# Performance work log

Hardware: AMD Instinct MI355X
Metric: run time of the kernel (lower is better)

## Reference

```python
import jax, jax.numpy as jnp
import numpy as np

B, K, HID, EMB = 16384, 8, 512, 512


def setup_inputs() -> dict:
    key = jax.random.key(0)
    ks = jax.random.split(key, 6)
    scale = 1.0 / np.sqrt(HID)
    return {
        "query": jax.random.normal(ks[0], (B, HID), jnp.float32),
        "topics": jax.random.normal(ks[1], (B, K, EMB), jnp.float32),
        "coverage_vector": jax.random.uniform(ks[2], (B, K), jnp.float32),
        "Ua_w": jax.random.normal(ks[3], (HID, EMB), jnp.float32) * scale,
        "Wa_w": jax.random.normal(ks[4], (HID, HID), jnp.float32) * scale,
        "va_w": jax.random.normal(ks[5], (HID,), jnp.float32) * scale,
        "va_b": jnp.zeros((1,), jnp.float32),
    }


def reference(query, topics, coverage_vector, Ua_w, Wa_w, va_w, va_b):
    # Faithful to the torch loop: query is re-projected by Wa EACH step,
    # so step i uses Wa^(i+1)(query) -- a sequential recurrence over K topics.
    # proj_key for all topics can be batched: [B,K,EMB] @ Ua_w.T -> [B,K,HID]
    proj_key = jnp.einsum('bke,he->bkh', topics, Ua_w)

    def step(q, pk_i):
        # q: [B,HID]; pk_i: [B,HID] (proj_key for topic i)
        q_new = q @ Wa_w.T
        s = jnp.tanh(q_new + pk_i) @ va_w + va_b[0]  # [B]
        return q_new, s

    # scan over the K topic steps (carry = evolving query)
    _, scores = jax.lax.scan(step, query, jnp.moveaxis(proj_key, 1, 0))
    scores = scores.T * coverage_vector  # [B,K]
    alphas = jax.nn.softmax(scores, axis=1)
    mt = jnp.einsum('bk,bke->be', alphas, topics)
    return mt, alphas
```

## Files before the change

kernel.cpp:

```cpp
#include <hip/hip_runtime.h>
#include <hip/hip_bf16.h>

#define HID 512
#define EMB 512
#define KTOP 8
#define BM 64
#define THREADS 1024
#define POWN (512 * 512)

typedef __attribute__((ext_vector_type(8))) short bf16x8;
typedef __attribute__((ext_vector_type(4))) float f32x4;
typedef __attribute__((ext_vector_type(4))) unsigned u32x4;

__device__ __forceinline__ short f2bf(float f) {
    unsigned u = __builtin_bit_cast(unsigned, f);
    u += 0x7fffu + ((u >> 16) & 1u);
    return (short)(u >> 16);
}
__device__ __forceinline__ float bf2f(short s) {
    unsigned u = ((unsigned)(unsigned short)s) << 16;
    return __builtin_bit_cast(float, u);
}
__device__ __forceinline__ unsigned cvtpk2(float x, float y) {
    return ((unsigned)(unsigned short)f2bf(x)) |
           (((unsigned)(unsigned short)f2bf(y)) << 16);
}
__device__ __forceinline__ bf16x8 pack8(f32x4 a, f32x4 b) {
    u32x4 r = {cvtpk2(a[0], a[1]), cvtpk2(a[2], a[3]),
               cvtpk2(b[0], b[1]), cvtpk2(b[2], b[3])};
    return __builtin_bit_cast(bf16x8, r);
}
__device__ __forceinline__ void split_bf(float w, short& hi, short& lo) {
    hi = f2bf(w);
    lo = f2bf(w - bf2f(hi));
}

__global__ void prep_kernel(const float* __restrict__ Wa, const float* __restrict__ Ua,
                            short* __restrict__ hiRM, short* __restrict__ loRM,
                            short* __restrict__ hiT, short* __restrict__ loT,
                            short* __restrict__ ua_b) {
    int i = blockIdx.x * blockDim.x + threadIdx.x;
    if (i >= POWN) return;
    int r = i >> 9, c = i & 511;
    short hi, lo;
    split_bf(Wa[i], hi, lo);
    hiRM[i] = hi; loRM[i] = lo;
    hiT[c * 512 + r] = hi;
    loT[c * 512 + r] = lo;
    ua_b[i] = f2bf(Ua[i]);
}

__device__ __forceinline__ int sel4(int4 v, int i) {
    int r = v.x;
    if (i == 1) r = v.y;
    if (i == 2) r = v.z;
    if (i == 3) r = v.w;
    return r;
}

__global__ __launch_bounds__(256)
void powmul_kernel(short* __restrict__ hiRM, short* __restrict__ loRM,
                   short* __restrict__ hiT, short* __restrict__ loT,
                   int4 aS, int4 bS, int4 dS) {
    const int p = blockIdx.z;
    const int as = sel4(aS, p), bs = sel4(bS, p), ds = sel4(dS, p);
    const short* Ah = hiRM + (size_t)as * POWN;
    const short* Al = loRM + (size_t)as * POWN;
    const short* Bh = hiT + (size_t)bs * POWN;
    const short* Bl = loT + (size_t)bs * POWN;

    const int tid = threadIdx.x, lane = tid & 63, w = tid >> 6;
    const int l15 = lane & 15, lg = lane >> 4;
    const int row = blockIdx.x * 64 + w * 16 + l15;
    const int colb = blockIdx.y * 64;

    f32x4 acc[4];
#pragma unroll
    for (int nf = 0; nf < 4; ++nf) acc[nf] = (f32x4){0.f, 0.f, 0.f, 0.f};

    for (int ch = 0; ch < 16; ++ch) {
        const int e0 = ch * 32 + lg * 8;
        bf16x8 ah = *(const bf16x8*)(Ah + row * 512 + e0);
        bf16x8 al = *(const bf16x8*)(Al + row * 512 + e0);
#pragma unroll
        for (int nf = 0; nf < 4; ++nf) {
            const int col = colb + nf * 16 + l15;
            bf16x8 bh = *(const bf16x8*)(Bh + col * 512 + e0);
            bf16x8 bl = *(const bf16x8*)(Bl + col * 512 + e0);
            acc[nf] = __builtin_amdgcn_mfma_f32_16x16x32_bf16(ah, bh, acc[nf], 0, 0, 0);
            acc[nf] = __builtin_amdgcn_mfma_f32_16x16x32_bf16(ah, bl, acc[nf], 0, 0, 0);
            acc[nf] = __builtin_amdgcn_mfma_f32_16x16x32_bf16(al, bh, acc[nf], 0, 0, 0);
        }
    }

    short* Dh = hiRM + (size_t)ds * POWN;
    short* Dl = loRM + (size_t)ds * POWN;
#pragma unroll
    for (int nf = 0; nf < 4; ++nf)
#pragma unroll
        for (int j = 0; j < 4; ++j) {
            int rg = blockIdx.x * 64 + w * 16 + lg * 4 + j;
            int cg = colb + nf * 16 + l15;
            short hi, lo;
            split_bf(acc[nf][j], hi, lo);
            Dh[rg * 512 + cg] = hi;
            Dl[rg * 512 + cg] = lo;
            if (ds < 4) {
                hiT[(size_t)ds * POWN + cg * 512 + rg] = hi;
                loT[(size_t)ds * POWN + cg * 512 + rg] = lo;
            }
        }
}

__global__ __launch_bounds__(256)
void swz_pow_kernel(const short* __restrict__ pow_hi, const short* __restrict__ pow_lo,
                    const short* __restrict__ ua_b,
                    short* __restrict__ swz_hi, short* __restrict__ swz_lo,
                    short* __restrict__ swz_ua) {
    const int m = blockIdx.y;
    const short* src;
    short* dst;
    if (m < 8)       { src = pow_hi + (size_t)m * POWN;       dst = swz_hi + (size_t)m * POWN; }
    else if (m < 16) { src = pow_lo + (size_t)(m - 8) * POWN; dst = swz_lo + (size_t)(m - 8) * POWN; }
    else             { src = ua_b;                             dst = swz_ua; }

#pragma unroll
    for (int i = 0; i < 8; ++i) {
        int c = blockIdx.x * 2048 + i * 256 + threadIdx.x;
        bf16x8 v = *(const bf16x8*)(src + c * 8);
        int ch = (c >> 2) & 15;
        int lg = c & 3;
        int cb = c >> 10;
        int l15 = (c >> 6) & 15;
        int lane = lg * 16 + l15;
        *(bf16x8*)(dst + ((size_t)(ch * 32 + cb) * 64 + lane) * 8) = v;
    }
}

__global__ __launch_bounds__(THREADS)
void q_prep_kernel(const float* __restrict__ query, short* __restrict__ q_sw) {
    __shared__ short q_s[BM * 512];
    const int tid = threadIdx.x;
    const long rbase = (long)blockIdx.x * BM;

#pragma unroll
    for (int i = 0; i < 4; ++i) {
        int idx = tid + i * THREADS;
        int r = idx >> 6, s = idx & 63;
        const float* qp = query + (rbase + r) * HID + s * 8;
        f32x4 a = *(const f32x4*)qp;
        f32x4 b = *(const f32x4*)(qp + 4);
        *(bf16x8*)&q_s[(r * 64 + (s ^ (r & 7))) * 8] = pack8(a, b);
    }
    __syncthreads();
    short* dst = q_sw + (size_t)blockIdx.x * (BM * 512);
#pragma unroll
    for (int i = 0; i < 4; ++i) {
        int d = tid + i * THREADS;
        int l15 = d & 15, lg = (d >> 4) & 3;
        int ch = (d >> 6) & 15, mf = (d >> 10) & 3;
        int r = mf * 16 + l15;
        int s = ch * 4 + lg;
        bf16x8 v = *(const bf16x8*)&q_s[(r * 64 + (s ^ (r & 7))) * 8];
        *(bf16x8*)(dst + (size_t)d * 8) = v;
    }
}

__global__ __launch_bounds__(THREADS, 4)
void attn_main_kernel(const float* __restrict__ topics,
                      const float* __restrict__ cov,
                      const short* __restrict__ q_sw,
                      const short* __restrict__ swz_hi,
                      const short* __restrict__ swz_lo,
                      const short* __restrict__ swz_ua,
                      const float* __restrict__ va_w,
                      const float* __restrict__ va_b,
                      float* __restrict__ out_mt,
                      float* __restrict__ out_alpha) {
    __shared__ short t_lds[BM * 512];
    __shared__ float scores_s[BM][KTOP];
    __shared__ float alpha_s[BM][KTOP];

    const int tid  = threadIdx.x;
    const int lane = tid & 63;
    const int wn   = tid >> 6;
    const int l15  = lane & 15;
    const int lg   = lane >> 4;
    const long rbase = (long)blockIdx.x * BM;

    if (tid < BM * KTOP) ((float*)scores_s)[tid] = 0.f;

    float va_reg[2];
#pragma unroll
    for (int nf = 0; nf < 2; ++nf) va_reg[nf] = va_w[wn * 32 + nf * 16 + l15];
    const float vab = va_b[0];

    const short* qbase = q_sw + (size_t)blockIdx.x * (BM * 512) + lane * 8;
    const int lane8 = lane * 8;

#pragma unroll 1
    for (int step = 0; step < KTOP; ++step) {
        __syncthreads();
#pragma unroll
        for (int i = 0; i < 4; ++i) {
            int idx = tid + i * THREADS;
            int r = idx >> 6, s = idx & 63;
            const float* tp = topics + ((rbase + r) * KTOP + step) * EMB + s * 8;
            f32x4 a = *(const f32x4*)tp;
            f32x4 b = *(const f32x4*)(tp + 4);
            *(bf16x8*)&t_lds[(r * 64 + (s ^ (r & 7))) * 8] = pack8(a, b);
        }
        __syncthreads();

        const short* wh = swz_hi + (size_t)step * POWN;
        const short* wl = swz_lo + (size_t)step * POWN;

        f32x4 acc[4][2];
#pragma unroll
        for (int mf = 0; mf < 4; ++mf)
#pragma unroll
            for (int nf = 0; nf < 2; ++nf) acc[mf][nf] = (f32x4){0.f, 0.f, 0.f, 0.f};

        for (int ch = 0; ch < 16; ++ch) {
            bf16x8 qf[4], tf[4];
#pragma unroll
            for (int mf = 0; mf < 4; ++mf) {
                qf[mf] = *(const bf16x8*)(qbase + (size_t)(mf * 16 + ch) * 512);
                int r = mf * 16 + l15;
                int s = ch * 4 + lg;
                tf[mf] = *(const bf16x8*)&t_lds[(r * 64 + (s ^ (r & 7))) * 8];
            }
#pragma unroll
            for (int nf = 0; nf < 2; ++nf) {
                const size_t off = (size_t)((ch * 32 + wn * 2 + nf) * 512 + lane8);
                bf16x8 bh = *(const bf16x8*)(wh + off);
                bf16x8 bl = *(const bf16x8*)(wl + off);
                bf16x8 bu = *(const bf16x8*)(swz_ua + off);
#pragma unroll
                for (int mf = 0; mf < 4; ++mf) {
                    acc[mf][nf] = __builtin_amdgcn_mfma_f32_16x16x32_bf16(qf[mf], bh, acc[mf][nf], 0, 0, 0);
                    acc[mf][nf] = __builtin_amdgcn_mfma_f32_16x16x32_bf16(qf[mf], bl, acc[mf][nf], 0, 0, 0);
                    acc[mf][nf] = __builtin_amdgcn_mfma_f32_16x16x32_bf16(tf[mf], bu, acc[mf][nf], 0, 0, 0);
                }
            }
        }

        float part[4][4];
#pragma unroll
        for (int mf = 0; mf < 4; ++mf)
#pragma unroll
            for (int j = 0; j < 4; ++j) part[mf][j] = 0.f;
#pragma unroll
        for (int mf = 0; mf < 4; ++mf)
#pragma unroll
            for (int nf = 0; nf < 2; ++nf)
#pragma unroll
                for (int j = 0; j < 4; ++j) {
                    float x = acc[mf][nf][j];
                    float e = __expf(2.f * x);
                    float th = 1.f - 2.f / (e + 1.f);
                    part[mf][j] += th * va_reg[nf];
                }
#pragma unroll
        for (int m = 8; m >= 1; m >>= 1)
#pragma unroll
            for (int mf = 0; mf < 4; ++mf)
#pragma unroll
                for (int j = 0; j < 4; ++j)
                    part[mf][j] += __shfl_xor(part[mf][j], m, 64);
        if (l15 == 0) {
#pragma unroll
            for (int mf = 0; mf < 4; ++mf)
#pragma unroll
                for (int j = 0; j < 4; ++j)
                    atomicAdd(&scores_s[mf * 16 + lg * 4 + j][step], part[mf][j]);
        }
    }

    __syncthreads();
    if (tid < BM * KTOP) {
        int r = tid >> 3, k = tid & 7;
        scores_s[r][k] = (scores_s[r][k] + vab) * cov[(rbase + r) * KTOP + k];
    }
    __syncthreads();
    if (tid < BM) {
        float mx = scores_s[tid][0];
#pragma unroll
        for (int k = 1; k < KTOP; ++k) mx = fmaxf(mx, scores_s[tid][k]);
        float e[KTOP], sum = 0.f;
#pragma unroll
        for (int k = 0; k < KTOP; ++k) { e[k] = __expf(scores_s[tid][k] - mx); sum += e[k]; }
#pragma unroll
        for (int k = 0; k < KTOP; ++k) {
            float a = e[k] / sum;
            alpha_s[tid][k] = a;
            out_alpha[(rbase + tid) * KTOP + k] = a;
        }
    }
    __syncthreads();

#pragma unroll 1
    for (int i = tid; i < BM * (EMB / 4); i += THREADS) {
        int r = i >> 7;
        int c4 = i & 127;
        const float* tb = topics + (rbase + r) * KTOP * EMB + c4 * 4;
        f32x4 acc = {0.f, 0.f, 0.f, 0.f};
#pragma unroll
        for (int k = 0; k < KTOP; ++k) {
            f32x4 t = *(const f32x4*)(tb + k * EMB);
            float a = alpha_s[r][k];
            acc[0] += t[0] * a;
            acc[1] += t[1] * a;
            acc[2] += t[2] * a;
            acc[3] += t[3] * a;
        }
        *(f32x4*)(out_mt + (rbase + r) * EMB + c4 * 4) = acc;
    }
}

extern "C" void kernel_launch(void* const* d_in, const int* in_sizes, int n_in,
                              void* d_out, int out_size, void* d_ws, size_t ws_size,
                              hipStream_t stream) {
    const float* query  = (const float*)d_in[0];
    const float* topics = (const float*)d_in[1];
    const float* cov    = (const float*)d_in[2];
    const float* Ua     = (const float*)d_in[3];
    const float* Wa     = (const float*)d_in[4];
    const float* va     = (const float*)d_in[5];
    const float* vab    = (const float*)d_in[6];

    const int Brows = in_sizes[0] / HID;
    const int nblk  = Brows / BM;

    short* pow_hi = (short*)d_ws;
    short* pow_lo = pow_hi + (size_t)8 * POWN;
    short* hiT    = pow_lo + (size_t)8 * POWN;
    short* loT    = hiT + (size_t)4 * POWN;
    short* ua_b   = loT + (size_t)4 * POWN;
    short* swz_hi = ua_b + POWN;
    short* swz_lo = swz_hi + (size_t)8 * POWN;
    short* swz_ua = swz_lo + (size_t)8 * POWN;
    short* q_sw   = swz_ua + POWN;

    float* out_mt    = (float*)d_out;
    float* out_alpha = out_mt + (size_t)Brows * EMB;

    prep_kernel<<<(POWN + 255) / 256, 256, 0, stream>>>(Wa, Ua, pow_hi, pow_lo,
                                                        hiT, loT, ua_b);
    powmul_kernel<<<dim3(8, 8, 1), 256, 0, stream>>>(pow_hi, pow_lo, hiT, loT,
        make_int4(0, 0, 0, 0), make_int4(0, 0, 0, 0), make_int4(1, 0, 0, 0));
    powmul_kernel<<<dim3(8, 8, 2), 256, 0, stream>>>(pow_hi, pow_lo, hiT, loT,
        make_int4(1, 1, 0, 0), make_int4(0, 1, 0, 0), make_int4(2, 3, 0, 0));
    powmul_kernel<<<dim3(8, 8, 4), 256, 0, stream>>>(pow_hi, pow_lo, hiT, loT,
        make_int4(3, 3, 2, 3), make_int4(0, 1, 3, 3), make_int4(4, 5, 6, 7));

    swz_pow_kernel<<<dim3(16, 17), 256, 0, stream>>>(pow_hi, pow_lo, ua_b,
                                                     swz_hi, swz_lo, swz_ua);
    q_prep_kernel<<<nblk, THREADS, 0, stream>>>(query, q_sw);

    attn_main_kernel<<<nblk, THREADS, 0, stream>>>(topics, cov, q_sw,
                                                   swz_hi, swz_lo, swz_ua,
                                                   va, vab, out_mt, out_alpha);
}
```

Before: 401.3 us.

## Double-buffer topic tiles and fuse online-softmax weighted sum into step loop

Topic tiles for the next step are prefetched into registers while the current step's MFMA work runs, then written to a second LDS buffer. The final mt computation no longer re-reads all topics from global memory. Instead, an online-softmax running sum over the bf16 topic tile already in LDS is kept in 32 registers per thread. This saves a full second pass over the topics tensor, but mt is now built from bf16-rounded topics, which costs accuracy. It also doubles LDS use and adds registers, which may hurt occupancy.

```diff
diff --git a/kernel.cpp b/kernel.cpp
--- a/kernel.cpp
+++ b/kernel.cpp
@@ -177,9 +177,8 @@
                       const float* __restrict__ va_b,
                       float* __restrict__ out_mt,
                       float* __restrict__ out_alpha) {
-    __shared__ short t_lds[BM * 512];
+    __shared__ short t_lds[2][BM * 512];
     __shared__ float scores_s[BM][KTOP];
-    __shared__ float alpha_s[BM][KTOP];
 
     const int tid  = threadIdx.x;
     const int lane = tid & 63;
@@ -195,22 +194,44 @@
     for (int nf = 0; nf < 2; ++nf) va_reg[nf] = va_w[wn * 32 + nf * 16 + l15];
     const float vab = va_b[0];
 
+    const int orow = tid >> 4;
+    const int oc0  = (tid & 15) * 32;
+    float o_acc[32];
+#pragma unroll
+    for (int j = 0; j < 32; ++j) o_acc[j] = 0.f;
+    float l_run = 0.f, m_run = -1e30f;
+
     const short* qbase = q_sw + (size_t)blockIdx.x * (BM * 512) + lane * 8;
     const int lane8 = lane * 8;
 
-#pragma unroll 1
-    for (int step = 0; step < KTOP; ++step) {
-        __syncthreads();
+    f32x4 sa[4], sb[4];
+    auto issue_stage = [&](int stp) {
 #pragma unroll
         for (int i = 0; i < 4; ++i) {
             int idx = tid + i * THREADS;
             int r = idx >> 6, s = idx & 63;
-            const float* tp = topics + ((rbase + r) * KTOP + step) * EMB + s * 8;
-            f32x4 a = *(const f32x4*)tp;
-            f32x4 b = *(const f32x4*)(tp + 4);
-            *(bf16x8*)&t_lds[(r * 64 + (s ^ (r & 7))) * 8] = pack8(a, b);
-        }
-        __syncthreads();
+            const float* tp = topics + ((rbase + r) * KTOP + stp) * EMB + s * 8;
+            sa[i] = *(const f32x4*)tp;
+            sb[i] = *(const f32x4*)(tp + 4);
+        }
+    };
+    auto write_stage = [&](int buf) {
+#pragma unroll
+        for (int i = 0; i < 4; ++i) {
+            int idx = tid + i * THREADS;
+            int r = idx >> 6, s = idx & 63;
+            *(bf16x8*)&t_lds[buf][(r * 64 + (s ^ (r & 7))) * 8] = pack8(sa[i], sb[i]);
+        }
+    };
+
+    issue_stage(0);
+    write_stage(0);
+    __syncthreads();
+
+#pragma unroll 1
+    for (int step = 0; step < KTOP; ++step) {
+        const int cur = step & 1;
+        if (step < KTOP - 1) issue_stage(step + 1);
 
         const short* wh = swz_hi + (size_t)step * POWN;
         const short* wl = swz_lo + (size_t)step * POWN;
@@ -228,7 +249,7 @@
                 qf[mf] = *(const bf16x8*)(qbase + (size_t)(mf * 16 + ch) * 512);
                 int r = mf * 16 + l15;
                 int s = ch * 4 + lg;
-                tf[mf] = *(const bf16x8*)&t_lds[(r * 64 + (s ^ (r & 7))) * 8];
+                tf[mf] = *(const bf16x8*)&t_lds[cur][(r * 64 + (s ^ (r & 7))) * 8];
             }
 #pragma unroll
             for (int nf = 0; nf < 2; ++nf) {
@@ -275,9 +296,32 @@
                 for (int j = 0; j < 4; ++j)
                     atomicAdd(&scores_s[mf * 16 + lg * 4 + j][step], part[mf][j]);
         }
-    }
-
-    __syncthreads();
+
+        __syncthreads();
+
+        {
+            float cv  = cov[(rbase + orow) * KTOP + step];
+            float s_k = (scores_s[orow][step] + vab) * cv;
+            float m_new = fmaxf(m_run, s_k);
+            float corr = __expf(m_run - m_new);
+            float w    = __expf(s_k - m_new);
+            l_run = l_run * corr + w;
+#pragma unroll
+            for (int u = 0; u < 4; ++u) {
+                int s = (oc0 >> 3) + u;
+                bf16x8 tv = *(const bf16x8*)&t_lds[cur][(orow * 64 + (s ^ (orow & 7))) * 8];
+#pragma unroll
+                for (int j = 0; j < 8; ++j)
+                    o_acc[u * 8 + j] = o_acc[u * 8 + j] * corr + w * bf2f(tv[j]);
+            }
+            m_run = m_new;
+        }
+
+        if (step < KTOP - 1) write_stage(cur ^ 1);
+
+        __syncthreads();
+    }
+
     if (tid < BM * KTOP) {
         int r = tid >> 3, k = tid & 7;
         scores_s[r][k] = (scores_s[r][k] + vab) * cov[(rbase + r) * KTOP + k];
@@ -291,30 +335,19 @@
 #pragma unroll
         for (int k = 0; k < KTOP; ++k) { e[k] = __expf(scores_s[tid][k] - mx); sum += e[k]; }
 #pragma unroll
-        for (int k = 0; k < KTOP; ++k) {
-            float a = e[k] / sum;
-            alpha_s[tid][k] = a;
-            out_alpha[(rbase + tid) * KTOP + k] = a;
-        }
-    }
-    __syncthreads();
-
-#pragma unroll 1
-    for (int i = tid; i < BM * (EMB / 4); i += THREADS) {
-        int r = i >> 7;
-        int c4 = i & 127;
-        const float* tb = topics + (rbase + r) * KTOP * EMB + c4 * 4;
-        f32x4 acc = {0.f, 0.f, 0.f, 0.f};
-#pragma unroll
-        for (int k = 0; k < KTOP; ++k) {
-            f32x4 t = *(const f32x4*)(tb + k * EMB);
-            float a = alpha_s[r][k];
-            acc[0] += t[0] * a;
-            acc[1] += t[1] * a;
-            acc[2] += t[2] * a;
-            acc[3] += t[3] * a;
-        }
-        *(f32x4*)(out_mt + (rbase + r) * EMB + c4 * 4) = acc;
+        for (int k = 0; k < KTOP; ++k)
+            out_alpha[(rbase + tid) * KTOP + k] = e[k] / sum;
+    }
+
+    {
+        float inv = 1.f / l_run;
+        float* mp = out_mt + (rbase + orow) * EMB + oc0;
+#pragma unroll
+        for (int u = 0; u < 8; ++u) {
+            f32x4 v = {o_acc[u * 4 + 0] * inv, o_acc[u * 4 + 1] * inv,
+                       o_acc[u * 4 + 2] * inv, o_acc[u * 4 + 3] * inv};
+            *(f32x4*)(mp + u * 4) = v;
+        }
     }
 }
 
```

Result: slower. 505.3 us (+25.9%).

## Split monolithic attention kernel into proj-key, scores, and weighted-sum kernels

Applied to the files above, without the earlier changes.

Replaces the single fused attention kernel with three kernels. The first computes the Ua projection of the topics and stores it in bf16 in a workspace buffer. The second runs the Wa-power MFMAs, tanh and softmax to produce alphas without holding topics in LDS. The third computes the alpha-weighted sum of topics. The aim is lower LDS and register pressure per kernel, paid for with extra global traffic: topics is read twice, and the bf16 projection is written and read back. The old fused kernel stays as a fallback when the workspace is too small.

```diff
diff --git a/kernel.cpp b/kernel.cpp
--- a/kernel.cpp
+++ b/kernel.cpp
@@ -9,6 +9,7 @@
 #define POWN (512 * 512)
 
 typedef __attribute__((ext_vector_type(8))) short bf16x8;
+typedef __attribute__((ext_vector_type(4))) short bf16x4;
 typedef __attribute__((ext_vector_type(4))) float f32x4;
 typedef __attribute__((ext_vector_type(4))) unsigned u32x4;
 
@@ -33,6 +34,10 @@
 __device__ __forceinline__ void split_bf(float w, short& hi, short& lo) {
     hi = f2bf(w);
     lo = f2bf(w - bf2f(hi));
+}
+
+__device__ __forceinline__ size_t pk_off(int blk, int step, int tid, int mf, int nf) {
+    return ((((size_t)blk * KTOP + step) * THREADS + tid) * 8 + mf * 2 + nf) * 4;
 }
 
 __global__ void prep_kernel(const float* __restrict__ Wa, const float* __restrict__ Ua,
@@ -167,7 +172,209 @@
 }
 
 __global__ __launch_bounds__(THREADS, 4)
-void attn_main_kernel(const float* __restrict__ topics,
+void pk_kernel(const float* __restrict__ topics,
+               const short* __restrict__ swz_ua,
+               short* __restrict__ pk) {
+    __shared__ short t_lds[BM * 512];
+    const int tid  = threadIdx.x;
+    const int lane = tid & 63;
+    const int wn   = tid >> 6;
+    const int l15  = lane & 15;
+    const int lg   = lane >> 4;
+    const long rbase = (long)blockIdx.x * BM;
+    const int lane8 = lane * 8;
+
+#pragma unroll 1
+    for (int step = 0; step < KTOP; ++step) {
+        __syncthreads();
+#pragma unroll
+        for (int i = 0; i < 4; ++i) {
+            int idx = tid + i * THREADS;
+            int r = idx >> 6, s = idx & 63;
+            const float* tp = topics + ((rbase + r) * KTOP + step) * EMB + s * 8;
+            f32x4 a = *(const f32x4*)tp;
+            f32x4 b = *(const f32x4*)(tp + 4);
+            *(bf16x8*)&t_lds[(r * 64 + (s ^ (r & 7))) * 8] = pack8(a, b);
+        }
+        __syncthreads();
+
+        f32x4 acc[4][2];
+#pragma unroll
+        for (int mf = 0; mf < 4; ++mf)
+#pragma unroll
+            for (int nf = 0; nf < 2; ++nf) acc[mf][nf] = (f32x4){0.f, 0.f, 0.f, 0.f};
+
+        for (int ch = 0; ch < 16; ++ch) {
+            bf16x8 tf[4];
+#pragma unroll
+            for (int mf = 0; mf < 4; ++mf) {
+                int r = mf * 16 + l15;
+                int s = ch * 4 + lg;
+                tf[mf] = *(const bf16x8*)&t_lds[(r * 64 + (s ^ (r & 7))) * 8];
+            }
+#pragma unroll
+            for (int nf = 0; nf < 2; ++nf) {
+                const size_t off = (size_t)((ch * 32 + wn * 2 + nf) * 512 + lane8);
+                bf16x8 bu = *(const bf16x8*)(swz_ua + off);
+#pragma unroll
+                for (int mf = 0; mf < 4; ++mf)
+                    acc[mf][nf] = __builtin_amdgcn_mfma_f32_16x16x32_bf16(tf[mf], bu, acc[mf][nf], 0, 0, 0);
+            }
+        }
+
+#pragma unroll
+        for (int mf = 0; mf < 4; ++mf)
+#pragma unroll
+            for (int nf = 0; nf < 2; ++nf) {
+                bf16x4 v = {f2bf(acc[mf][nf][0]), f2bf(acc[mf][nf][1]),
+                            f2bf(acc[mf][nf][2]), f2bf(acc[mf][nf][3])};
+                *(bf16x4*)(pk + pk_off(blockIdx.x, step, tid, mf, nf)) = v;
+            }
+    }
+}
+
+__global__ __launch_bounds__(THREADS, 4)
+void attn_scores_kernel(const float* __restrict__ cov,
+                        const short* __restrict__ q_sw,
+                        const short* __restrict__ swz_hi,
+                        const short* __restrict__ swz_lo,
+                        const short* __restrict__ pk,
+                        const float* __restrict__ va_w,
+                        const float* __restrict__ va_b,
+                        float* __restrict__ out_alpha) {
+    __shared__ float scores_s[BM][KTOP];
+
+    const int tid  = threadIdx.x;
+    const int lane = tid & 63;
+    const int wn   = tid >> 6;
+    const int l15  = lane & 15;
+    const int lg   = lane >> 4;
+    const long rbase = (long)blockIdx.x * BM;
+    const int lane8 = lane * 8;
+
+    if (tid < BM * KTOP) ((float*)scores_s)[tid] = 0.f;
+
+    float va_reg[2];
+#pragma unroll
+    for (int nf = 0; nf < 2; ++nf) va_reg[nf] = va_w[wn * 32 + nf * 16 + l15];
+    const float vab = va_b[0];
+
+    const short* qbase = q_sw + (size_t)blockIdx.x * (BM * 512) + lane * 8;
+
+    __syncthreads();
+
+#pragma unroll 1
+    for (int step = 0; step < KTOP; ++step) {
+        const short* wh = swz_hi + (size_t)step * POWN;
+        const short* wl = swz_lo + (size_t)step * POWN;
+
+        f32x4 acc[4][2];
+#pragma unroll
+        for (int mf = 0; mf < 4; ++mf)
+#pragma unroll
+            for (int nf = 0; nf < 2; ++nf) acc[mf][nf] = (f32x4){0.f, 0.f, 0.f, 0.f};
+
+        for (int ch = 0; ch < 16; ++ch) {
+            bf16x8 qf[4];
+#pragma unroll
+            for (int mf = 0; mf < 4; ++mf)
+                qf[mf] = *(const bf16x8*)(qbase + (size_t)(mf * 16 + ch) * 512);
+#pragma unroll
+            for (int nf = 0; nf < 2; ++nf) {
+                const size_t off = (size_t)((ch * 32 + wn * 2 + nf) * 512 + lane8);
+                bf16x8 bh = *(const bf16x8*)(wh + off);
+                bf16x8 bl = *(const bf16x8*)(wl + off);
+#pragma unroll
+                for (int mf = 0; mf < 4; ++mf) {
+                    acc[mf][nf] = __builtin_amdgcn_mfma_f32_16x16x32_bf16(qf[mf], bh, acc[mf][nf], 0, 0, 0);
+                    acc[mf][nf] = __builtin_amdgcn_mfma_f32_16x16x32_bf16(qf[mf], bl, acc[mf][nf], 0, 0, 0);
+                }
+            }
+        }
+
+        float part[4][4];
+#pragma unroll
+        for (int mf = 0; mf < 4; ++mf)
+#pragma unroll
+            for (int j = 0; j < 4; ++j) part[mf][j] = 0.f;
+#pragma unroll
+        for (int mf = 0; mf < 4; ++mf)
+#pragma unroll
+            for (int nf = 0; nf < 2; ++nf) {
+                bf16x4 pv = *(const bf16x4*)(pk + pk_off(blockIdx.x, step, tid, mf, nf));
+#pragma unroll
+                for (int j = 0; j < 4; ++j) {
+                    float x = acc[mf][nf][j] + bf2f(pv[j]);
+                    float e = __expf(2.f * x);
+                    float th = 1.f - 2.f / (e + 1.f);
+                    part[mf][j] += th * va_reg[nf];
+                }
+            }
+#pragma unroll
+        for (int m = 8; m >= 1; m >>= 1)
+#pragma unroll
+            for (int mf = 0; mf < 4; ++mf)
+#pragma unroll
+                for (int j = 0; j < 4; ++j)
+                    part[mf][j] += __shfl_xor(part[mf][j], m, 64);
+        if (l15 == 0) {
+#pragma unroll
+            for (int mf = 0; mf < 4; ++mf)
+#pragma unroll
+                for (int j = 0; j < 4; ++j)
+                    atomicAdd(&scores_s[mf * 16 + lg * 4 + j][step], part[mf][j]);
+        }
+    }
+
+    __syncthreads();
+    if (tid < BM * KTOP) {
+        int r = tid >> 3, k = tid & 7;
+        scores_s[r][k] = (scores_s[r][k] + vab) * cov[(rbase + r) * KTOP + k];
+    }
+    __syncthreads();
+    if (tid < BM) {
+        float mx = scores_s[tid][0];
+#pragma unroll
+        for (int k = 1; k < KTOP; ++k) mx = fmaxf(mx, scores_s[tid][k]);
+        float e[KTOP], sum = 0.f;
+#pragma unroll
+        for (int k = 0; k < KTOP; ++k) { e[k] = __expf(scores_s[tid][k] - mx); sum += e[k]; }
+#pragma unroll
+        for (int k = 0; k < KTOP; ++k)
+            out_alpha[(rbase + tid) * KTOP + k] = e[k] / sum;
+    }
+}
+
+__global__ __launch_bounds__(256)
+void mt_kernel(const float* __restrict__ topics, const float* __restrict__ alphas,
+               float* __restrict__ out_mt) {
+    int idx = blockIdx.x * 256 + threadIdx.x;
+    int r  = idx >> 5;
+    int c0 = (idx & 31) * 16;
+    float a[KTOP];
+#pragma unroll
+    for (int k = 0; k < KTOP; ++k) a[k] = alphas[(size_t)r * KTOP + k];
+    const float* tb = topics + (size_t)r * KTOP * EMB + c0;
+    f32x4 o[4];
+#pragma unroll
+    for (int u = 0; u < 4; ++u) o[u] = (f32x4){0.f, 0.f, 0.f, 0.f};
+#pragma unroll
+    for (int k = 0; k < KTOP; ++k)
+#pragma unroll
+        for (int u = 0; u < 4; ++u) {
+            f32x4 t = *(const f32x4*)(tb + k * EMB + u * 4);
+            o[u][0] += a[k] * t[0];
+            o[u][1] += a[k] * t[1];
+            o[u][2] += a[k] * t[2];
+            o[u][3] += a[k] * t[3];
+        }
+    float* mp = out_mt + (size_t)r * EMB + c0;
+#pragma unroll
+    for (int u = 0; u < 4; ++u) *(f32x4*)(mp + u * 4) = o[u];
+}
+
+__global__ __launch_bounds__(THREADS, 4)
+void attn_mono_kernel(const float* __restrict__ topics,
                       const float* __restrict__ cov,
                       const short* __restrict__ q_sw,
                       const short* __restrict__ swz_hi,
@@ -341,6 +548,10 @@
     short* swz_lo = swz_hi + (size_t)8 * POWN;
     short* swz_ua = swz_lo + (size_t)8 * POWN;
     short* q_sw   = swz_ua + POWN;
+    short* pk     = q_sw + (size_t)Brows * 512;
+
+    const size_t need = ((size_t)(25 + 17) * POWN + (size_t)Brows * 512 +
+                         (size_t)nblk * KTOP * THREADS * 32) * sizeof(short);
 
     float* out_mt    = (float*)d_out;
     float* out_alpha = out_mt + (size_t)Brows * EMB;
@@ -358,7 +569,14 @@
                                                      swz_hi, swz_lo, swz_ua);
     q_prep_kernel<<<nblk, THREADS, 0, stream>>>(query, q_sw);
 
-    attn_main_kernel<<<nblk, THREADS, 0, stream>>>(topics, cov, q_sw,
-                                                   swz_hi, swz_lo, swz_ua,
-                                                   va, vab, out_mt, out_alpha);
-}
+    if (ws_size >= need) {
+        pk_kernel<<<nblk, THREADS, 0, stream>>>(topics, swz_ua, pk);
+        attn_scores_kernel<<<nblk, THREADS, 0, stream>>>(cov, q_sw, swz_hi, swz_lo,
+                                                         pk, va, vab, out_alpha);
+        mt_kernel<<<(Brows * EMB / 16) / 256, 256, 0, stream>>>(topics, out_alpha, out_mt);
+    } else {
+        attn_mono_kernel<<<nblk, THREADS, 0, stream>>>(topics, cov, q_sw,
+                                                       swz_hi, swz_lo, swz_ua,
+                                                       va, vab, out_mt, out_alpha);
+    }
+}
```

New measurement: 1.113 ms. 177% more time.

## Switch main GEMMs to fp16 single-pass and double-buffer topic tiles

Applied to the files above, without the earlier changes.

Replaces the bf16 hi/lo split of the Wa powers with a single fp16 weight (hi+lo rounded to fp16), and converts query, topics and Ua to fp16. This cuts the main-loop MFMA count from three to two per fragment and halves the Wa weight traffic. It also double-buffers the per-step topic tile in shared memory so the next step's global loads are issued before the current step's compute. The risks are fp16 range and precision limits on the Wa powers and activations, and doubled LDS use, which may cut occupancy.

```diff
diff --git a/kernel.cpp b/kernel.cpp
--- a/kernel.cpp
+++ b/kernel.cpp
@@ -9,6 +9,7 @@
 #define POWN (512 * 512)
 
 typedef __attribute__((ext_vector_type(8))) short bf16x8;
+typedef __attribute__((ext_vector_type(8))) _Float16 f16x8;
 typedef __attribute__((ext_vector_type(4))) float f32x4;
 typedef __attribute__((ext_vector_type(4))) unsigned u32x4;
 
@@ -21,24 +22,22 @@
     unsigned u = ((unsigned)(unsigned short)s) << 16;
     return __builtin_bit_cast(float, u);
 }
-__device__ __forceinline__ unsigned cvtpk2(float x, float y) {
-    return ((unsigned)(unsigned short)f2bf(x)) |
-           (((unsigned)(unsigned short)f2bf(y)) << 16);
-}
-__device__ __forceinline__ bf16x8 pack8(f32x4 a, f32x4 b) {
-    u32x4 r = {cvtpk2(a[0], a[1]), cvtpk2(a[2], a[3]),
-               cvtpk2(b[0], b[1]), cvtpk2(b[2], b[3])};
-    return __builtin_bit_cast(bf16x8, r);
-}
 __device__ __forceinline__ void split_bf(float w, short& hi, short& lo) {
     hi = f2bf(w);
     lo = f2bf(w - bf2f(hi));
 }
-
-__global__ void prep_kernel(const float* __restrict__ Wa, const float* __restrict__ Ua,
+__device__ __forceinline__ f16x8 pack8h(f32x4 a, f32x4 b) {
+    f16x8 r;
+    r[0] = (_Float16)a[0]; r[1] = (_Float16)a[1];
+    r[2] = (_Float16)a[2]; r[3] = (_Float16)a[3];
+    r[4] = (_Float16)b[0]; r[5] = (_Float16)b[1];
+    r[6] = (_Float16)b[2]; r[7] = (_Float16)b[3];
+    return r;
+}
+
+__global__ void prep_kernel(const float* __restrict__ Wa,
                             short* __restrict__ hiRM, short* __restrict__ loRM,
-                            short* __restrict__ hiT, short* __restrict__ loT,
-                            short* __restrict__ ua_b) {
+                            short* __restrict__ hiT, short* __restrict__ loT) {
     int i = blockIdx.x * blockDim.x + threadIdx.x;
     if (i >= POWN) return;
     int r = i >> 9, c = i & 511;
@@ -47,7 +46,6 @@
     hiRM[i] = hi; loRM[i] = lo;
     hiT[c * 512 + r] = hi;
     loT[c * 512 + r] = lo;
-    ua_b[i] = f2bf(Ua[i]);
 }
 
 __device__ __forceinline__ int sel4(int4 v, int i) {
@@ -113,27 +111,34 @@
 }
 
 __global__ __launch_bounds__(256)
-void swz_pow_kernel(const short* __restrict__ pow_hi, const short* __restrict__ pow_lo,
-                    const short* __restrict__ ua_b,
-                    short* __restrict__ swz_hi, short* __restrict__ swz_lo,
-                    short* __restrict__ swz_ua) {
+void swz_cvt_kernel(const short* __restrict__ pow_hi, const short* __restrict__ pow_lo,
+                    const float* __restrict__ Ua,
+                    short* __restrict__ swz_w, short* __restrict__ swz_ua) {
     const int m = blockIdx.y;
-    const short* src;
-    short* dst;
-    if (m < 8)       { src = pow_hi + (size_t)m * POWN;       dst = swz_hi + (size_t)m * POWN; }
-    else if (m < 16) { src = pow_lo + (size_t)(m - 8) * POWN; dst = swz_lo + (size_t)(m - 8) * POWN; }
-    else             { src = ua_b;                             dst = swz_ua; }
-
 #pragma unroll
     for (int i = 0; i < 8; ++i) {
         int c = blockIdx.x * 2048 + i * 256 + threadIdx.x;
-        bf16x8 v = *(const bf16x8*)(src + c * 8);
+        f16x8 v;
+        if (m < 8) {
+            const short* hs = pow_hi + (size_t)m * POWN + c * 8;
+            const short* ls = pow_lo + (size_t)m * POWN + c * 8;
+            bf16x8 h = *(const bf16x8*)hs;
+            bf16x8 l = *(const bf16x8*)ls;
+#pragma unroll
+            for (int j = 0; j < 8; ++j) v[j] = (_Float16)(bf2f(h[j]) + bf2f(l[j]));
+        } else {
+            const float* up = Ua + (size_t)(c >> 6) * 512 + (c & 63) * 8;
+            f32x4 a = *(const f32x4*)up;
+            f32x4 b = *(const f32x4*)(up + 4);
+            v = pack8h(a, b);
+        }
         int ch = (c >> 2) & 15;
         int lg = c & 3;
         int cb = c >> 10;
         int l15 = (c >> 6) & 15;
         int lane = lg * 16 + l15;
-        *(bf16x8*)(dst + ((size_t)(ch * 32 + cb) * 64 + lane) * 8) = v;
+        short* dst = (m < 8) ? (swz_w + (size_t)m * POWN) : swz_ua;
+        *(f16x8*)(dst + ((size_t)(ch * 32 + cb) * 64 + lane) * 8) = v;
     }
 }
 
@@ -150,7 +155,7 @@
         const float* qp = query + (rbase + r) * HID + s * 8;
         f32x4 a = *(const f32x4*)qp;
         f32x4 b = *(const f32x4*)(qp + 4);
-        *(bf16x8*)&q_s[(r * 64 + (s ^ (r & 7))) * 8] = pack8(a, b);
+        *(f16x8*)&q_s[(r * 64 + (s ^ (r & 7))) * 8] = pack8h(a, b);
     }
     __syncthreads();
     short* dst = q_sw + (size_t)blockIdx.x * (BM * 512);
@@ -161,8 +166,8 @@
         int ch = (d >> 6) & 15, mf = (d >> 10) & 3;
         int r = mf * 16 + l15;
         int s = ch * 4 + lg;
-        bf16x8 v = *(const bf16x8*)&q_s[(r * 64 + (s ^ (r & 7))) * 8];
-        *(bf16x8*)(dst + (size_t)d * 8) = v;
+        f16x8 v = *(const f16x8*)&q_s[(r * 64 + (s ^ (r & 7))) * 8];
+        *(f16x8*)(dst + (size_t)d * 8) = v;
     }
 }
 
@@ -170,14 +175,13 @@
 void attn_main_kernel(const float* __restrict__ topics,
                       const float* __restrict__ cov,
                       const short* __restrict__ q_sw,
-                      const short* __restrict__ swz_hi,
-                      const short* __restrict__ swz_lo,
+                      const short* __restrict__ swz_w,
                       const short* __restrict__ swz_ua,
                       const float* __restrict__ va_w,
                       const float* __restrict__ va_b,
                       float* __restrict__ out_mt,
                       float* __restrict__ out_alpha) {
-    __shared__ short t_lds[BM * 512];
+    __shared__ short t_lds[2][BM * 512];
     __shared__ float scores_s[BM][KTOP];
     __shared__ float alpha_s[BM][KTOP];
 
@@ -198,22 +202,36 @@
     const short* qbase = q_sw + (size_t)blockIdx.x * (BM * 512) + lane * 8;
     const int lane8 = lane * 8;
 
-#pragma unroll 1
-    for (int step = 0; step < KTOP; ++step) {
-        __syncthreads();
+    f32x4 sa[4], sb[4];
+    auto issue_stage = [&](int stp) {
 #pragma unroll
         for (int i = 0; i < 4; ++i) {
             int idx = tid + i * THREADS;
             int r = idx >> 6, s = idx & 63;
-            const float* tp = topics + ((rbase + r) * KTOP + step) * EMB + s * 8;
-            f32x4 a = *(const f32x4*)tp;
-            f32x4 b = *(const f32x4*)(tp + 4);
-            *(bf16x8*)&t_lds[(r * 64 + (s ^ (r & 7))) * 8] = pack8(a, b);
-        }
-        __syncthreads();
-
-        const short* wh = swz_hi + (size_t)step * POWN;
-        const short* wl = swz_lo + (size_t)step * POWN;
+            const float* tp = topics + ((rbase + r) * KTOP + stp) * EMB + s * 8;
+            sa[i] = *(const f32x4*)tp;
+            sb[i] = *(const f32x4*)(tp + 4);
+        }
+    };
+    auto write_stage = [&](int buf) {
+#pragma unroll
+        for (int i = 0; i < 4; ++i) {
+            int idx = tid + i * THREADS;
+            int r = idx >> 6, s = idx & 63;
+            *(f16x8*)&t_lds[buf][(r * 64 + (s ^ (r & 7))) * 8] = pack8h(sa[i], sb[i]);
+        }
+    };
+
+    issue_stage(0);
+    write_stage(0);
+    __syncthreads();
+
+#pragma unroll 1
+    for (int step = 0; step < KTOP; ++step) {
+        const int cur = step & 1;
+        if (step < KTOP - 1) issue_stage(step + 1);
+
+        const short* wh = swz_w + (size_t)step * POWN;
 
         f32x4 acc[4][2];
 #pragma unroll
@@ -222,25 +240,23 @@
             for (int nf = 0; nf < 2; ++nf) acc[mf][nf] = (f32x4){0.f, 0.f, 0.f, 0.f};
 
         for (int ch = 0; ch < 16; ++ch) {
-            bf16x8 qf[4], tf[4];
+            f16x8 qf[4], tf[4];
 #pragma unroll
             for (int mf = 0; mf < 4; ++mf) {
-                qf[mf] = *(const bf16x8*)(qbase + (size_t)(mf * 16 + ch) * 512);
+                qf[mf] = *(const f16x8*)(qbase + (size_t)(mf * 16 + ch) * 512);
                 int r = mf * 16 + l15;
                 int s = ch * 4 + lg;
-                tf[mf] = *(const bf16x8*)&t_lds[(r * 64 + (s ^ (r & 7))) * 8];
+                tf[mf] = *(const f16x8*)&t_lds[cur][(r * 64 + (s ^ (r & 7))) * 8];
             }
 #pragma unroll
             for (int nf = 0; nf < 2; ++nf) {
                 const size_t off = (size_t)((ch * 32 + wn * 2 + nf) * 512 + lane8);
-                bf16x8 bh = *(const bf16x8*)(wh + off);
-                bf16x8 bl = *(const bf16x8*)(wl + off);
-                bf16x8 bu = *(const bf16x8*)(swz_ua + off);
+                f16x8 bw = *(const f16x8*)(wh + off);
+                f16x8 bu = *(const f16x8*)(swz_ua + off);
 #pragma unroll
                 for (int mf = 0; mf < 4; ++mf) {
-                    acc[mf][nf] = __builtin_amdgcn_mfma_f32_16x16x32_bf16(qf[mf], bh, acc[mf][nf], 0, 0, 0);
-                    acc[mf][nf] = __builtin_amdgcn_mfma_f32_16x16x32_bf16(qf[mf], bl, acc[mf][nf], 0, 0, 0);
-                    acc[mf][nf] = __builtin_amdgcn_mfma_f32_16x16x32_bf16(tf[mf], bu, acc[mf][nf], 0, 0, 0);
+                    acc[mf][nf] = __builtin_amdgcn_mfma_f32_16x16x32_f16(qf[mf], bw, acc[mf][nf], 0, 0, 0);
+                    acc[mf][nf] = __builtin_amdgcn_mfma_f32_16x16x32_f16(tf[mf], bu, acc[mf][nf], 0, 0, 0);
                 }
             }
         }
@@ -275,9 +291,12 @@
                 for (int j = 0; j < 4; ++j)
                     atomicAdd(&scores_s[mf * 16 + lg * 4 + j][step], part[mf][j]);
         }
-    }
-
-    __syncthreads();
+
+        __syncthreads();
+        if (step < KTOP - 1) write_stage(cur ^ 1);
+        __syncthreads();
+    }
+
     if (tid < BM * KTOP) {
         int r = tid >> 3, k = tid & 7;
         scores_s[r][k] = (scores_s[r][k] + vab) * cov[(rbase + r) * KTOP + k];
@@ -336,17 +355,14 @@
     short* pow_lo = pow_hi + (size_t)8 * POWN;
     short* hiT    = pow_lo + (size_t)8 * POWN;
     short* loT    = hiT + (size_t)4 * POWN;
-    short* ua_b   = loT + (size_t)4 * POWN;
-    short* swz_hi = ua_b + POWN;
-    short* swz_lo = swz_hi + (size_t)8 * POWN;
-    short* swz_ua = swz_lo + (size_t)8 * POWN;
+    short* swz_w  = loT + (size_t)4 * POWN;
+    short* swz_ua = swz_w + (size_t)8 * POWN;
     short* q_sw   = swz_ua + POWN;
 
     float* out_mt    = (float*)d_out;
     float* out_alpha = out_mt + (size_t)Brows * EMB;
 
-    prep_kernel<<<(POWN + 255) / 256, 256, 0, stream>>>(Wa, Ua, pow_hi, pow_lo,
-                                                        hiT, loT, ua_b);
+    prep_kernel<<<(POWN + 255) / 256, 256, 0, stream>>>(Wa, pow_hi, pow_lo, hiT, loT);
     powmul_kernel<<<dim3(8, 8, 1), 256, 0, stream>>>(pow_hi, pow_lo, hiT, loT,
         make_int4(0, 0, 0, 0), make_int4(0, 0, 0, 0), make_int4(1, 0, 0, 0));
     powmul_kernel<<<dim3(8, 8, 2), 256, 0, stream>>>(pow_hi, pow_lo, hiT, loT,
@@ -354,11 +370,10 @@
     powmul_kernel<<<dim3(8, 8, 4), 256, 0, stream>>>(pow_hi, pow_lo, hiT, loT,
         make_int4(3, 3, 2, 3), make_int4(0, 1, 3, 3), make_int4(4, 5, 6, 7));
 
-    swz_pow_kernel<<<dim3(16, 17), 256, 0, stream>>>(pow_hi, pow_lo, ua_b,
-                                                     swz_hi, swz_lo, swz_ua);
+    swz_cvt_kernel<<<dim3(16, 9), 256, 0, stream>>>(pow_hi, pow_lo, Ua, swz_w, swz_ua);
     q_prep_kernel<<<nblk, THREADS, 0, stream>>>(query, q_sw);
 
     attn_main_kernel<<<nblk, THREADS, 0, stream>>>(topics, cov, q_sw,
-                                                   swz_hi, swz_lo, swz_ua,
+                                                   swz_w, swz_ua,
                                                    va, vab, out_mt, out_alpha);
 }
```

Measured after the change: 1.253 ms. +212.1%, slower.
